# Optimization experiments

Measured on AMD Instinct MI355X. Metric: run time of the kernel, lower is better.

Reference implementation:

```python
import jax, jax.numpy as jnp
import numpy as np

B, S, E = 2, 2048, 2048
N_HEAD = 16
HEAD_DIM = E // N_HEAD  # 128
MP_NUM = 4              # hardcoded in the torch forward
ROTARY_DIM = 64


def setup_inputs() -> dict:
    key = jax.random.key(0)
    k1, k2, k3 = jax.random.split(key, 3)
    return {
        "hidden_states": jax.random.normal(k1, (B, S, E), jnp.float32) * 0.02,
        "w_qkv": jax.random.normal(k2, (3 * E, E), jnp.float32) * 0.02,  # torch Linear weight [out,in]
        "w_out": jax.random.normal(k3, (E, E), jnp.float32) * 0.02,
    }


def _rotate_every_two(x):
    # (..., d) -> interleaved (-x2, x1) as in GPT-J/CodeGen
    x1 = x[..., 0::2]
    x2 = x[..., 1::2]
    return jnp.stack((-x2, x1), axis=-1).reshape(x.shape)


def reference(hidden_states, w_qkv, w_out):
    b, s, e = hidden_states.shape
    local = e // MP_NUM  # per-mp-shard channel count

    # qkv projection (no bias), then mp_num split: order is (query, value, key)
    qkv = jnp.einsum("bse,fe->bsf", hidden_states, w_qkv)  # [B,S,3E]
    qkv = qkv.reshape(b, s, MP_NUM, 3 * local)
    q = qkv[..., :local].reshape(b, s, N_HEAD, HEAD_DIM)
    v = qkv[..., local:2 * local].reshape(b, s, N_HEAD, HEAD_DIM)
    k = qkv[..., 2 * local:].reshape(b, s, N_HEAD, HEAD_DIM)

    # partial rotary (rotate-every-two) on first ROTARY_DIM channels
    inv_freq = 1.0 / (10000.0 ** (jnp.arange(0, ROTARY_DIM, 2, dtype=jnp.float32) / ROTARY_DIM))
    freqs = jnp.arange(s, dtype=jnp.float32)[:, None] * inv_freq[None, :]  # [S, R/2]
    sin = jnp.repeat(jnp.sin(freqs), 2, axis=-1)[None, :, None, :]  # [1,S,1,R]
    cos = jnp.repeat(jnp.cos(freqs), 2, axis=-1)[None, :, None, :]

    def rope(x):
        x_rot = x[..., :ROTARY_DIM]
        x_pass = x[..., ROTARY_DIM:]
        x_rot = x_rot * cos + _rotate_every_two(x_rot) * sin
        return jnp.concatenate([x_rot, x_pass], axis=-1)

    q = rope(q)
    k = rope(k)

    # [B,S,H,D] -> [B,H,S,D]
    q = q.transpose(0, 2, 1, 3)
    k = k.transpose(0, 2, 1, 3)
    v = v.transpose(0, 2, 1, 3)

    scale = jnp.sqrt(jnp.asarray(HEAD_DIM, dtype=q.dtype))
    scores = jnp.einsum("bhqd,bhkd->bhqk", q, k) / scale  # [B,H,S,S]
    causal = jnp.tril(jnp.ones((s, s), dtype=bool))
    scores = jnp.where(causal[None, None, :, :], scores, jnp.finfo(scores.dtype).min)
    attn = jax.nn.softmax(scores, axis=-1)

    out = jnp.einsum("bhqk,bhkd->bhqd", attn, v)  # [B,H,S,D]
    out = out.transpose(0, 2, 1, 3).reshape(b, s, e)  # merge heads
    return jnp.einsum("bse,fe->bsf", out, w_out)  # out_proj (no bias)
```

## Files before the change

### kernel.cpp

```cpp
#include <hip/hip_runtime.h>

typedef unsigned short u16;
typedef unsigned int u32;
typedef __attribute__((ext_vector_type(4))) float f32x4;
typedef __attribute__((ext_vector_type(8))) short s16x8;
typedef __attribute__((ext_vector_type(4))) unsigned int u32x4;

#define DEVI static __device__ __forceinline__


#define ROPE_C (-13.287712379549449f / 32.0f)
#define QSCALE 0.12751743f

DEVI u16 f2bf(float f) {
  u32 u = __float_as_uint(f);
  return (u16)((u + 0x7FFFu + ((u >> 16) & 1u)) >> 16);
}
DEVI float bf2f(u16 h) { return __uint_as_float(((u32)h) << 16); }

DEVI void async_copy16(const u16* g, u16* l) {
  __builtin_amdgcn_global_load_lds((__attribute__((address_space(1))) void*)g,
                                   (__attribute__((address_space(3))) void*)l, 16, 0, 0);
}

__global__ __launch_bounds__(256) void cast3_kernel(
    const float* __restrict__ s0, u16* __restrict__ d0, int n0,
    const float* __restrict__ s1, u16* __restrict__ d1, int n1,
    const float* __restrict__ s2, u16* __restrict__ d2, int n2) {
  int i = blockIdx.x * 256 + threadIdx.x;
  const float* s;
  u16* d;
  if (i < n0) {
    s = s0; d = d0;
  } else if (i < n0 + n1) {
    s = s1; d = d1; i -= n0;
  } else if (i < n0 + n1 + n2) {
    s = s2; d = d2; i -= n0 + n1;
  } else {
    return;
  }
  const float4 v = ((const float4*)s)[i];
  ushort4 o;
  o.x = f2bf(v.x); o.y = f2bf(v.y); o.z = f2bf(v.z); o.w = f2bf(v.w);
  ((ushort4*)d)[i] = o;
}

template <int EPI>
__global__ __launch_bounds__(256, 3) void gemm_bt_kernel(
    const u16* __restrict__ A, const u16* __restrict__ Bm, int K, int N,
    float* __restrict__ C, u16* __restrict__ qo, u16* __restrict__ ko, u16* __restrict__ vo) {
  __shared__ __attribute__((aligned(16))) u16 As[3][128 * 32];
  __shared__ __attribute__((aligned(16))) u16 Bs[3][128 * 32];
  const int tid = threadIdx.x;
  const int w = tid >> 6, lane = tid & 63;
  const int quad = lane >> 4, l16 = lane & 15;
  const int wrow = (w >> 1) * 64, wcol = (w & 1) * 64;
  const long tileM = (long)blockIdx.y * 128;
  const long tileN = (long)blockIdx.x * 128;

  f32x4 acc[4][4];
#pragma unroll
  for (int i = 0; i < 4; ++i)
#pragma unroll
    for (int j = 0; j < 4; ++j) acc[i][j] = f32x4{0.f, 0.f, 0.f, 0.f};

  const u16* aptr[2];
  const u16* bptr[2];
  int ldso[2];
#pragma unroll
  for (int c = 0; c < 2; ++c) {
    const int r0 = (w * 2 + c) * 16;
    const int row = r0 + (lane >> 2);
    const int colsw = (((lane & 3) ^ ((row >> 1) & 3)) << 3);
    aptr[c] = A + (tileM + row) * (long)K + colsw;
    bptr[c] = Bm + (tileN + row) * (long)K + colsw;
    ldso[c] = r0 * 32;
  }

  auto stage = [&](int k0, int buf) {
#pragma unroll
    for (int c = 0; c < 2; ++c) {
      async_copy16(aptr[c] + k0, &As[buf][ldso[c]]);
      async_copy16(bptr[c] + k0, &Bs[buf][ldso[c]]);
    }
  };

  stage(0, 0);
  stage(32, 1);

  const int psw = (quad ^ ((l16 >> 1) & 3)) << 3;

  int bt = 0;
  for (int k0 = 0; k0 < K; k0 += 32) {
    if (k0 + 32 < K)
      __builtin_amdgcn_s_waitcnt(0x0f74);
    else
      __builtin_amdgcn_s_waitcnt(0x0f70);
    __builtin_amdgcn_s_barrier();
    if (k0 + 64 < K) stage(k0 + 64, bt == 0 ? 2 : bt - 1);

    s16x8 af[4], bfr[4];
#pragma unroll
    for (int i = 0; i < 4; ++i)
      af[i] = *(const s16x8*)(&As[bt][(wrow + i * 16 + l16) * 32 + psw]);
#pragma unroll
    for (int j = 0; j < 4; ++j)
      bfr[j] = *(const s16x8*)(&Bs[bt][(wcol + j * 16 + l16) * 32 + psw]);
#pragma unroll
    for (int i = 0; i < 4; ++i)
#pragma unroll
      for (int j = 0; j < 4; ++j)
        acc[i][j] = __builtin_amdgcn_mfma_f32_16x16x32_bf16(af[i], bfr[j], acc[i][j], 0, 0, 0);
    bt = bt == 2 ? 0 : bt + 1;
  }

  const int b = (int)(tileM >> 11);
#pragma unroll
  for (int i = 0; i < 4; ++i) {
#pragma unroll
    for (int j = 0; j < 4; ++j) {
      const int rowb = (int)((tileM + wrow + i * 16 + quad * 4) & 2047);
      if (EPI == 0) {
#pragma unroll
        for (int r = 0; r < 4; ++r) {
          const long row = tileM + wrow + i * 16 + quad * 4 + r;
          C[row * N + tileN + wcol + j * 16 + l16] = acc[i][j][r];
        }
      } else {
        const long col0 = tileN + wcol + j * 16;
        const int mp = (int)(col0 / 1536);
        const int cc0 = (int)(col0 - (long)mp * 1536);
        const int part = cc0 >> 9;
        const int idx0 = cc0 & 511;
        const int head = mp * 4 + (idx0 >> 7);
        const int dim0 = idx0 & 127;
        const int dim = dim0 + l16;
        const long bh = (long)(b * 16 + head);
        if (part == 1) {
#pragma unroll
          for (int r = 0; r < 4; ++r)
            vo[(bh * 128 + dim) * 2048 + rowb + r] = f2bf(acc[i][j][r]);
        } else {
          float y[4];
          if (part == 2 && dim0 < 64) {
            const int jj = dim >> 1;
            const float inv = exp2f((float)jj * ROPE_C);
#pragma unroll
            for (int r = 0; r < 4; ++r) {
              const float v = acc[i][j][r];
              const float pv = __shfl_xor(v, 1, 64);
              const float ang = (float)(rowb + r) * inv;
              const float sn = __sinf(ang), cs = __cosf(ang);
              y[r] = (l16 & 1) ? (v * cs + pv * sn) : (v * cs - pv * sn);
            }
          } else {
#pragma unroll
            for (int r = 0; r < 4; ++r) y[r] = acc[i][j][r];
          }
          u16* dst = (part == 0) ? qo : ko;
#pragma unroll
          for (int r = 0; r < 4; ++r)
            dst[(bh * 2048 + rowb + r) * 128 + dim] = f2bf(y[r]);
        }
      }
    }
  }
}

__global__ __launch_bounds__(256, 4) void attn_kernel(
    const u16* __restrict__ q, const u16* __restrict__ k,
    const u16* __restrict__ vT, u16* __restrict__ out) {
  __shared__ __attribute__((aligned(16))) u16 Ks[2][32 * 128];
  __shared__ __attribute__((aligned(16))) u16 Vs[2][128 * 32];
  const int tid = threadIdx.x;
  const int w = tid >> 6, lane = tid & 63;
  const int quad = lane >> 4, l16 = lane & 15;
  const int qt = 31 - (blockIdx.x >> 5);
  const int bh = blockIdx.x & 31;
  const int qbase = qt * 64 + w * 16;

  const u16* qp = q + ((long)bh * 2048 + qbase) * 128;
  const u16* kp = k + (long)bh * 2048 * 128;
  const u16* vp = vT + (long)bh * 128 * 2048;

  const float spos = (float)(qbase + l16);
  s16x8 qf[4];
#pragma unroll
  for (int c = 0; c < 4; ++c) {
    const s16x8 raw = *(const s16x8*)(qp + l16 * 128 + c * 32 + quad * 8);
    s16x8 ov;
    if (c < 2) {
#pragma unroll
      for (int m = 0; m < 4; ++m) {
        const int jj = c * 16 + quad * 4 + m;
        const float inv = exp2f((float)jj * ROPE_C);
        const float ang = spos * inv;
        const float sn = __sinf(ang), cs = __cosf(ang);
        const float x0 = bf2f((u16)raw[2 * m]), x1 = bf2f((u16)raw[2 * m + 1]);
        ov[2 * m] = (short)f2bf((x0 * cs - x1 * sn) * QSCALE);
        ov[2 * m + 1] = (short)f2bf((x1 * cs + x0 * sn) * QSCALE);
      }
    } else {
#pragma unroll
      for (int e = 0; e < 8; ++e) ov[e] = (short)f2bf(bf2f((u16)raw[e]) * QSCALE);
    }
    qf[c] = ov;
  }

  f32x4 acc[8];
#pragma unroll
  for (int d = 0; d < 8; ++d) acc[d] = f32x4{0.f, 0.f, 0.f, 0.f};
  float mrun = -1e30f, lrun = 0.f;

  auto stage = [&](int k0, int buf) {
    const int ko = lane >> 4, cl = lane & 15;
#pragma unroll
    for (int i = 0; i < 2; ++i) {
      const int keyt = w * 8 + i * 4;
      const int key = keyt + ko;
      async_copy16(kp + (long)(k0 + key) * 128 + ((cl ^ (key & 15)) << 3),
                   &Ks[buf][keyt * 128]);
    }
    const int ld = lane >> 2, c4 = lane & 3;
#pragma unroll
    for (int i = 0; i < 2; ++i) {
      const int db = w * 32 + i * 16;
      const int d = db + ld;
      async_copy16(vp + (long)d * 2048 + k0 + ((c4 ^ ((d >> 1) & 3)) << 3),
                   &Vs[buf][db * 32]);
    }
  };

  stage(0, 0);

  const int nt = 2 * qt + 2;
  for (int t = 0; t < nt; ++t) {
    const int k0 = t * 32;
    const u16* Ksc = Ks[t & 1];
    const u16* Vsc = Vs[t & 1];
    __builtin_amdgcn_s_waitcnt(0x0f70);
    __syncthreads();
    if (t + 1 < nt) stage(k0 + 32, (t + 1) & 1);

    f32x4 sc[2];
#pragma unroll
    for (int g = 0; g < 2; ++g) {
      sc[g] = f32x4{0.f, 0.f, 0.f, 0.f};
#pragma unroll
      for (int c = 0; c < 4; ++c) {
        const s16x8 kf = *(const s16x8*)(
            &Ksc[(g * 16 + l16) * 128 + ((((c << 2) + quad) ^ l16) << 3)]);
        sc[g] = __builtin_amdgcn_mfma_f32_16x16x32_bf16(kf, qf[c], sc[g], 0, 0, 0);
      }
    }
    if (k0 + 31 > qbase) {
      const int qrow = qbase + l16;
#pragma unroll
      for (int g = 0; g < 2; ++g) {
        const int keyb = k0 + g * 16 + quad * 4;
#pragma unroll
        for (int r = 0; r < 4; ++r)
          if (keyb + r > qrow) sc[g][r] = -1e30f;
      }
    }
    float mx = fmaxf(fmaxf(fmaxf(sc[0][0], sc[0][1]), fmaxf(sc[0][2], sc[0][3])),
                     fmaxf(fmaxf(sc[1][0], sc[1][1]), fmaxf(sc[1][2], sc[1][3])));
    mx = fmaxf(mx, __shfl_xor(mx, 16, 64));
    mx = fmaxf(mx, __shfl_xor(mx, 32, 64));
    const float mnew = fmaxf(mrun, mx);
    const float alpha = exp2f(mrun - mnew);
    mrun = mnew;
    float p[2][4];
    float sm = 0.f;
#pragma unroll
    for (int g = 0; g < 2; ++g)
#pragma unroll
      for (int r = 0; r < 4; ++r) { p[g][r] = exp2f(sc[g][r] - mnew); sm += p[g][r]; }
    sm += __shfl_xor(sm, 16, 64);
    sm += __shfl_xor(sm, 32, 64);
    lrun = lrun * alpha + sm;
#pragma unroll
    for (int d = 0; d < 8; ++d)
#pragma unroll
      for (int r = 0; r < 4; ++r) acc[d][r] *= alpha;

    u32 pk[2][2];
#pragma unroll
    for (int g = 0; g < 2; ++g) {
      pk[g][0] = (u32)f2bf(p[g][0]) | ((u32)f2bf(p[g][1]) << 16);
      pk[g][1] = (u32)f2bf(p[g][2]) | ((u32)f2bf(p[g][3]) << 16);
    }
    const int la = ((quad & 1) << 5) + l16;
    const int lb = la + 16;
    const u32 a0 = (u32)__shfl((int)pk[0][0], la, 64);
    const u32 a1 = (u32)__shfl((int)pk[0][1], la, 64);
    const u32 a2 = (u32)__shfl((int)pk[0][0], lb, 64);
    const u32 a3 = (u32)__shfl((int)pk[0][1], lb, 64);
    const u32 b0 = (u32)__shfl((int)pk[1][0], la, 64);
    const u32 b1 = (u32)__shfl((int)pk[1][1], la, 64);
    const u32 b2 = (u32)__shfl((int)pk[1][0], lb, 64);
    const u32 b3 = (u32)__shfl((int)pk[1][1], lb, 64);
    const bool hi = quad >= 2;
    const u32x4 pw = {hi ? b0 : a0, hi ? b1 : a1, hi ? b2 : a2, hi ? b3 : a3};
    const s16x8 pf = __builtin_bit_cast(s16x8, pw);

#pragma unroll
    for (int dd = 0; dd < 8; ++dd) {
      const s16x8 vf = *(const s16x8*)(
          &Vsc[(dd * 16 + l16) * 32 + ((quad ^ ((l16 >> 1) & 3)) << 3)]);
      acc[dd] = __builtin_amdgcn_mfma_f32_16x16x32_bf16(vf, pf, acc[dd], 0, 0, 0);
    }
  }

  const int b = bh >> 4, h = bh & 15;
  u16* op = out + ((long)b * 2048 + qbase + l16) * 2048 + h * 128;
  const float inv_l = 1.0f / lrun;
#pragma unroll
  for (int dd = 0; dd < 8; ++dd) {
    ushort4 o4;
    o4.x = f2bf(acc[dd][0] * inv_l);
    o4.y = f2bf(acc[dd][1] * inv_l);
    o4.z = f2bf(acc[dd][2] * inv_l);
    o4.w = f2bf(acc[dd][3] * inv_l);
    *(ushort4*)(op + dd * 16 + quad * 4) = o4;
  }
}

extern "C" void kernel_launch(void* const* d_in, const int* in_sizes, int n_in,
                              void* d_out, int out_size, void* d_ws, size_t ws_size,
                              hipStream_t stream) {
  const float* hidden = (const float*)d_in[0];
  const float* w_qkv = (const float*)d_in[1];
  const float* w_out = (const float*)d_in[2];
  float* out = (float*)d_out;
  char* ws = (char*)d_ws;

  u16* hid_b  = (u16*)(ws + (size_t)0);
  u16* wqkv_b = (u16*)(ws + (size_t)16777216);
  u16* wout_b = (u16*)(ws + (size_t)41943040);
  u16* qb     = (u16*)(ws + (size_t)50331648);
  u16* kb     = (u16*)(ws + (size_t)67108864);
  u16* vb     = (u16*)(ws + (size_t)83886080);
  u16* ao     = (u16*)(ws + (size_t)100663296);

  cast3_kernel<<<24576, 256, 0, stream>>>(hidden, hid_b, 2097152,
                                          w_qkv, wqkv_b, 3145728,
                                          w_out, wout_b, 1048576);

  gemm_bt_kernel<1><<<dim3(48, 32), 256, 0, stream>>>(hid_b, wqkv_b, 2048, 6144,
                                                      nullptr, qb, kb, vb);
  attn_kernel<<<1024, 256, 0, stream>>>(qb, kb, vb, ao);
  gemm_bt_kernel<0><<<dim3(16, 32), 256, 0, stream>>>(ao, wout_b, 2048, 2048,
                                                      out, nullptr, nullptr, nullptr);
}
```

Baseline: 382.3 us.

## Process two 16-row query tiles per wave in attention to reuse K/V fragments

Each wave now handles 32 query rows (two 16-row sub-tiles) instead of 16, so every block covers 128 queries and the grid halves to 512 blocks. Each K and V fragment read from shared memory feeds two MFMAs, which halves LDS traffic and global K/V staging per query. Waves skip key tiles entirely above their causal diagonal. In exchange, register pressure doubles for accumulators, occupancy drops (launch bounds 4 to 3), there are fewer blocks, and causal load imbalance within a block grows.

```diff
diff --git a/kernel.cpp b/kernel.cpp
--- a/kernel.cpp
+++ b/kernel.cpp
@@ -167,7 +167,7 @@
   }
 }
 
-__global__ __launch_bounds__(256, 4) void attn_kernel(
+__global__ __launch_bounds__(256, 3) void attn_kernel(
     const u16* __restrict__ q, const u16* __restrict__ k,
     const u16* __restrict__ vT, u16* __restrict__ out) {
   __shared__ __attribute__((aligned(16))) u16 Ks[2][32 * 128];
@@ -175,42 +175,47 @@
   const int tid = threadIdx.x;
   const int w = tid >> 6, lane = tid & 63;
   const int quad = lane >> 4, l16 = lane & 15;
-  const int qt = 31 - (blockIdx.x >> 5);
+  const int qt = 15 - (blockIdx.x >> 5);
   const int bh = blockIdx.x & 31;
-  const int qbase = qt * 64 + w * 16;
-
-  const u16* qp = q + ((long)bh * 2048 + qbase) * 128;
+  const int qb0 = qt * 128 + w * 32;
+
+  const u16* qp = q + ((long)bh * 2048 + qb0) * 128;
   const u16* kp = k + (long)bh * 2048 * 128;
   const u16* vp = vT + (long)bh * 128 * 2048;
 
-  const float spos = (float)(qbase + l16);
-  s16x8 qf[4];
-#pragma unroll
-  for (int c = 0; c < 4; ++c) {
-    const s16x8 raw = *(const s16x8*)(qp + l16 * 128 + c * 32 + quad * 8);
-    s16x8 ov;
-    if (c < 2) {
-#pragma unroll
-      for (int m = 0; m < 4; ++m) {
-        const int jj = c * 16 + quad * 4 + m;
-        const float inv = exp2f((float)jj * ROPE_C);
-        const float ang = spos * inv;
-        const float sn = __sinf(ang), cs = __cosf(ang);
-        const float x0 = bf2f((u16)raw[2 * m]), x1 = bf2f((u16)raw[2 * m + 1]);
-        ov[2 * m] = (short)f2bf((x0 * cs - x1 * sn) * QSCALE);
-        ov[2 * m + 1] = (short)f2bf((x1 * cs + x0 * sn) * QSCALE);
-      }
-    } else {
-#pragma unroll
-      for (int e = 0; e < 8; ++e) ov[e] = (short)f2bf(bf2f((u16)raw[e]) * QSCALE);
-    }
-    qf[c] = ov;
-  }
-
-  f32x4 acc[8];
-#pragma unroll
-  for (int d = 0; d < 8; ++d) acc[d] = f32x4{0.f, 0.f, 0.f, 0.f};
-  float mrun = -1e30f, lrun = 0.f;
+  s16x8 qf[2][4];
+#pragma unroll
+  for (int u = 0; u < 2; ++u) {
+    const float spos = (float)(qb0 + u * 16 + l16);
+#pragma unroll
+    for (int c = 0; c < 4; ++c) {
+      const s16x8 raw = *(const s16x8*)(qp + (u * 16 + l16) * 128 + c * 32 + quad * 8);
+      s16x8 ov;
+      if (c < 2) {
+#pragma unroll
+        for (int m = 0; m < 4; ++m) {
+          const int jj = c * 16 + quad * 4 + m;
+          const float inv = exp2f((float)jj * ROPE_C);
+          const float ang = spos * inv;
+          const float sn = __sinf(ang), cs = __cosf(ang);
+          const float x0 = bf2f((u16)raw[2 * m]), x1 = bf2f((u16)raw[2 * m + 1]);
+          ov[2 * m] = (short)f2bf((x0 * cs - x1 * sn) * QSCALE);
+          ov[2 * m + 1] = (short)f2bf((x1 * cs + x0 * sn) * QSCALE);
+        }
+      } else {
+#pragma unroll
+        for (int e = 0; e < 8; ++e) ov[e] = (short)f2bf(bf2f((u16)raw[e]) * QSCALE);
+      }
+      qf[u][c] = ov;
+    }
+  }
+
+  f32x4 acc[2][8];
+#pragma unroll
+  for (int u = 0; u < 2; ++u)
+#pragma unroll
+    for (int d = 0; d < 8; ++d) acc[u][d] = f32x4{0.f, 0.f, 0.f, 0.f};
+  float mrun[2] = {-1e30f, -1e30f}, lrun[2] = {0.f, 0.f};
 
   auto stage = [&](int k0, int buf) {
     const int ko = lane >> 4, cl = lane & 15;
@@ -233,7 +238,8 @@
 
   stage(0, 0);
 
-  const int nt = 2 * qt + 2;
+  const int nt = 4 * qt + 4;
+  const int tmax = 4 * qt + w;
   for (int t = 0; t < nt; ++t) {
     const int k0 = t * 32;
     const u16* Ksc = Ks[t & 1];
@@ -241,88 +247,101 @@
     __builtin_amdgcn_s_waitcnt(0x0f70);
     __syncthreads();
     if (t + 1 < nt) stage(k0 + 32, (t + 1) & 1);
-
-    f32x4 sc[2];
-#pragma unroll
-    for (int g = 0; g < 2; ++g) {
-      sc[g] = f32x4{0.f, 0.f, 0.f, 0.f};
+    if (t > tmax) continue;
+
+    f32x4 sc[2][2];
+#pragma unroll
+    for (int u = 0; u < 2; ++u)
+#pragma unroll
+      for (int g = 0; g < 2; ++g) sc[u][g] = f32x4{0.f, 0.f, 0.f, 0.f};
+#pragma unroll
+    for (int g = 0; g < 2; ++g)
 #pragma unroll
       for (int c = 0; c < 4; ++c) {
         const s16x8 kf = *(const s16x8*)(
             &Ksc[(g * 16 + l16) * 128 + ((((c << 2) + quad) ^ l16) << 3)]);
-        sc[g] = __builtin_amdgcn_mfma_f32_16x16x32_bf16(kf, qf[c], sc[g], 0, 0, 0);
-      }
-    }
-    if (k0 + 31 > qbase) {
-      const int qrow = qbase + l16;
+        sc[0][g] = __builtin_amdgcn_mfma_f32_16x16x32_bf16(kf, qf[0][c], sc[0][g], 0, 0, 0);
+        sc[1][g] = __builtin_amdgcn_mfma_f32_16x16x32_bf16(kf, qf[1][c], sc[1][g], 0, 0, 0);
+      }
+
+    s16x8 pf[2];
+#pragma unroll
+    for (int u = 0; u < 2; ++u) {
+      if (k0 + 31 > qb0 + u * 16) {
+        const int qrow = qb0 + u * 16 + l16;
+#pragma unroll
+        for (int g = 0; g < 2; ++g) {
+          const int keyb = k0 + g * 16 + quad * 4;
+#pragma unroll
+          for (int r = 0; r < 4; ++r)
+            if (keyb + r > qrow) sc[u][g][r] = -1e30f;
+        }
+      }
+      float mx = fmaxf(fmaxf(fmaxf(sc[u][0][0], sc[u][0][1]), fmaxf(sc[u][0][2], sc[u][0][3])),
+                       fmaxf(fmaxf(sc[u][1][0], sc[u][1][1]), fmaxf(sc[u][1][2], sc[u][1][3])));
+      mx = fmaxf(mx, __shfl_xor(mx, 16, 64));
+      mx = fmaxf(mx, __shfl_xor(mx, 32, 64));
+      const float mnew = fmaxf(mrun[u], mx);
+      const float alpha = exp2f(mrun[u] - mnew);
+      mrun[u] = mnew;
+      float p[2][4];
+      float sm = 0.f;
+#pragma unroll
+      for (int g = 0; g < 2; ++g)
+#pragma unroll
+        for (int r = 0; r < 4; ++r) { p[g][r] = exp2f(sc[u][g][r] - mnew); sm += p[g][r]; }
+      sm += __shfl_xor(sm, 16, 64);
+      sm += __shfl_xor(sm, 32, 64);
+      lrun[u] = lrun[u] * alpha + sm;
+#pragma unroll
+      for (int d = 0; d < 8; ++d)
+#pragma unroll
+        for (int r = 0; r < 4; ++r) acc[u][d][r] *= alpha;
+
+      u32 pk[2][2];
 #pragma unroll
       for (int g = 0; g < 2; ++g) {
-        const int keyb = k0 + g * 16 + quad * 4;
-#pragma unroll
-        for (int r = 0; r < 4; ++r)
-          if (keyb + r > qrow) sc[g][r] = -1e30f;
-      }
-    }
-    float mx = fmaxf(fmaxf(fmaxf(sc[0][0], sc[0][1]), fmaxf(sc[0][2], sc[0][3])),
-                     fmaxf(fmaxf(sc[1][0], sc[1][1]), fmaxf(sc[1][2], sc[1][3])));
-    mx = fmaxf(mx, __shfl_xor(mx, 16, 64));
-    mx = fmaxf(mx, __shfl_xor(mx, 32, 64));
-    const float mnew = fmaxf(mrun, mx);
-    const float alpha = exp2f(mrun - mnew);
-    mrun = mnew;
-    float p[2][4];
-    float sm = 0.f;
-#pragma unroll
-    for (int g = 0; g < 2; ++g)
-#pragma unroll
-      for (int r = 0; r < 4; ++r) { p[g][r] = exp2f(sc[g][r] - mnew); sm += p[g][r]; }
-    sm += __shfl_xor(sm, 16, 64);
-    sm += __shfl_xor(sm, 32, 64);
-    lrun = lrun * alpha + sm;
-#pragma unroll
-    for (int d = 0; d < 8; ++d)
-#pragma unroll
-      for (int r = 0; r < 4; ++r) acc[d][r] *= alpha;
-
-    u32 pk[2][2];
-#pragma unroll
-    for (int g = 0; g < 2; ++g) {
-      pk[g][0] = (u32)f2bf(p[g][0]) | ((u32)f2bf(p[g][1]) << 16);
-      pk[g][1] = (u32)f2bf(p[g][2]) | ((u32)f2bf(p[g][3]) << 16);
-    }
-    const int la = ((quad & 1) << 5) + l16;
-    const int lb = la + 16;
-    const u32 a0 = (u32)__shfl((int)pk[0][0], la, 64);
-    const u32 a1 = (u32)__shfl((int)pk[0][1], la, 64);
-    const u32 a2 = (u32)__shfl((int)pk[0][0], lb, 64);
-    const u32 a3 = (u32)__shfl((int)pk[0][1], lb, 64);
-    const u32 b0 = (u32)__shfl((int)pk[1][0], la, 64);
-    const u32 b1 = (u32)__shfl((int)pk[1][1], la, 64);
-    const u32 b2 = (u32)__shfl((int)pk[1][0], lb, 64);
-    const u32 b3 = (u32)__shfl((int)pk[1][1], lb, 64);
-    const bool hi = quad >= 2;
-    const u32x4 pw = {hi ? b0 : a0, hi ? b1 : a1, hi ? b2 : a2, hi ? b3 : a3};
-    const s16x8 pf = __builtin_bit_cast(s16x8, pw);
+        pk[g][0] = (u32)f2bf(p[g][0]) | ((u32)f2bf(p[g][1]) << 16);
+        pk[g][1] = (u32)f2bf(p[g][2]) | ((u32)f2bf(p[g][3]) << 16);
+      }
+      const int la = ((quad & 1) << 5) + l16;
+      const int lb = la + 16;
+      const u32 a0 = (u32)__shfl((int)pk[0][0], la, 64);
+      const u32 a1 = (u32)__shfl((int)pk[0][1], la, 64);
+      const u32 a2 = (u32)__shfl((int)pk[0][0], lb, 64);
+      const u32 a3 = (u32)__shfl((int)pk[0][1], lb, 64);
+      const u32 b0 = (u32)__shfl((int)pk[1][0], la, 64);
+      const u32 b1 = (u32)__shfl((int)pk[1][1], la, 64);
+      const u32 b2 = (u32)__shfl((int)pk[1][0], lb, 64);
+      const u32 b3 = (u32)__shfl((int)pk[1][1], lb, 64);
+      const bool hi = quad >= 2;
+      const u32x4 pw = {hi ? b0 : a0, hi ? b1 : a1, hi ? b2 : a2, hi ? b3 : a3};
+      pf[u] = __builtin_bit_cast(s16x8, pw);
+    }
 
 #pragma unroll
     for (int dd = 0; dd < 8; ++dd) {
       const s16x8 vf = *(const s16x8*)(
           &Vsc[(dd * 16 + l16) * 32 + ((quad ^ ((l16 >> 1) & 3)) << 3)]);
-      acc[dd] = __builtin_amdgcn_mfma_f32_16x16x32_bf16(vf, pf, acc[dd], 0, 0, 0);
+      acc[0][dd] = __builtin_amdgcn_mfma_f32_16x16x32_bf16(vf, pf[0], acc[0][dd], 0, 0, 0);
+      acc[1][dd] = __builtin_amdgcn_mfma_f32_16x16x32_bf16(vf, pf[1], acc[1][dd], 0, 0, 0);
     }
   }
 
   const int b = bh >> 4, h = bh & 15;
-  u16* op = out + ((long)b * 2048 + qbase + l16) * 2048 + h * 128;
-  const float inv_l = 1.0f / lrun;
-#pragma unroll
-  for (int dd = 0; dd < 8; ++dd) {
-    ushort4 o4;
-    o4.x = f2bf(acc[dd][0] * inv_l);
-    o4.y = f2bf(acc[dd][1] * inv_l);
-    o4.z = f2bf(acc[dd][2] * inv_l);
-    o4.w = f2bf(acc[dd][3] * inv_l);
-    *(ushort4*)(op + dd * 16 + quad * 4) = o4;
+#pragma unroll
+  for (int u = 0; u < 2; ++u) {
+    u16* op = out + ((long)b * 2048 + qb0 + u * 16 + l16) * 2048 + h * 128;
+    const float inv_l = 1.0f / lrun[u];
+#pragma unroll
+    for (int dd = 0; dd < 8; ++dd) {
+      ushort4 o4;
+      o4.x = f2bf(acc[u][dd][0] * inv_l);
+      o4.y = f2bf(acc[u][dd][1] * inv_l);
+      o4.z = f2bf(acc[u][dd][2] * inv_l);
+      o4.w = f2bf(acc[u][dd][3] * inv_l);
+      *(ushort4*)(op + dd * 16 + quad * 4) = o4;
+    }
   }
 }
 
@@ -349,7 +368,7 @@
 
   gemm_bt_kernel<1><<<dim3(48, 32), 256, 0, stream>>>(hid_b, wqkv_b, 2048, 6144,
                                                       nullptr, qb, kb, vb);
-  attn_kernel<<<1024, 256, 0, stream>>>(qb, kb, vb, ao);
+  attn_kernel<<<512, 256, 0, stream>>>(qb, kb, vb, ao);
   gemm_bt_kernel<0><<<dim3(16, 32), 256, 0, stream>>>(ao, wout_b, 2048, 2048,
                                                       out, nullptr, nullptr, nullptr);
 }
```

Result: slower. 413.2 us (+8.1%).
